# Optimization experiments

Measured on AMD Instinct MI355X. Metric: run time of the kernel, lower is better.

Reference implementation:

```python
import jax, jax.numpy as jnp
import numpy as np

B, H, S, D = 8, 16, 1024, 128

def setup_inputs() -> dict:
    key = jax.random.key(0)
    kq, kk, kv = jax.random.split(key, 3)
    q = jax.random.normal(kq, (B, H, S, D), dtype=jnp.float32)
    k = jax.random.normal(kk, (B, H, S, D), dtype=jnp.float32)
    v = jax.random.normal(kv, (B, H, S, D), dtype=jnp.float32)
    return {"q": q, "k": k, "v": v}

def reference(q, k, v):
    dims = q.shape[-1]
    # scores[..., j, i] = sum_k q[..., j, k] * k_[..., i, k]; note scale is 1/dims (not 1/sqrt(dims))
    scores = jnp.einsum('bhjd,bhid->bhji', q, k) / dims
    probs = jax.nn.softmax(scores, axis=-1)
    out = jnp.einsum('bhji,bhid->bhjd', probs, v)
    return out
```

## Files before the change

### kernel.cpp

```cpp
#include <hip/hip_runtime.h>

#define S_LEN 1024
#define D_DIM 128
#define KVBLK 64
#define QROWS_BLK 128
#define BH_N 128
#define M0_LOG2 2.0f

typedef __attribute__((ext_vector_type(8))) short short8;
typedef __attribute__((ext_vector_type(4))) short short4v;
typedef __attribute__((ext_vector_type(4))) float f32x4;

__device__ __forceinline__ unsigned short f2bf(float f) {
  union { float f; unsigned u; } x; x.f = f;
  unsigned r = x.u + 0x7fffu + ((x.u >> 16) & 1u);
  return (unsigned short)(r >> 16);
}

__device__ __forceinline__ short8 pack8(float4 a, float4 b) {
  short8 f;
  f[0] = (short)f2bf(a.x); f[1] = (short)f2bf(a.y);
  f[2] = (short)f2bf(a.z); f[3] = (short)f2bf(a.w);
  f[4] = (short)f2bf(b.x); f[5] = (short)f2bf(b.y);
  f[6] = (short)f2bf(b.z); f[7] = (short)f2bf(b.w);
  return f;
}

__device__ __forceinline__ void gload_lds16(const void* g, void* l) {
  __builtin_amdgcn_global_load_lds(
      (const __attribute__((address_space(1))) unsigned int*)g,
      (__attribute__((address_space(3))) unsigned int*)l, 16, 0, 0);
}

__global__ __launch_bounds__(256) void conv_k(const float* __restrict__ in,
                                              unsigned short* __restrict__ out,
                                              int n8) {
  int i = blockIdx.x * 256 + threadIdx.x;
  int stride = gridDim.x * 256;
  for (; i < n8; i += stride) {
    float4 a = ((const float4*)in)[i * 2];
    float4 b = ((const float4*)in)[i * 2 + 1];
    ((short8*)out)[i] = pack8(a, b);
  }
}

__global__ __launch_bounds__(256) void conv_vt(const float* __restrict__ v,
                                               unsigned short* __restrict__ vt) {
  __shared__ unsigned short tile[64][72];
  int b = blockIdx.x;
  int d0 = (b & 1) * 64;
  int s0 = ((b >> 1) & 15) * 64;
  int bh = b >> 5;
  int t = threadIdx.x;
  #pragma unroll
  for (int i = 0; i < 4; ++i) {
    int s = (t >> 4) + i * 16;
    int dl = (t & 15) * 4;
    float4 x = *(const float4*)(v + ((size_t)(bh * S_LEN) + s0 + s) * D_DIM + d0 + dl);
    tile[s][dl + 0] = f2bf(x.x); tile[s][dl + 1] = f2bf(x.y);
    tile[s][dl + 2] = f2bf(x.z); tile[s][dl + 3] = f2bf(x.w);
  }
  __syncthreads();
  #pragma unroll
  for (int i = 0; i < 2; ++i) {
    int j = i * 256 + t;
    int dl = j >> 3, sc = j & 7;
    short8 w;
    #pragma unroll
    for (int q = 0; q < 8; ++q) w[q] = (short)tile[sc * 8 + q][dl];
    *(short8*)(vt + ((size_t)(bh * D_DIM) + d0 + dl) * S_LEN + s0 + sc * 8) = w;
  }
}

__global__ __launch_bounds__(512, 4) void attn_main(
    const float* __restrict__ qg, const unsigned short* __restrict__ kbf,
    const unsigned short* __restrict__ vtbf, float* __restrict__ og) {
  __shared__ unsigned short K_lds[2][KVBLK * D_DIM];
  __shared__ unsigned short VT_lds[2][D_DIM * KVBLK];
  __shared__ unsigned short P_lds[8][16 * KVBLK];

  const int tid = threadIdx.x;
  const int lane = tid & 63;
  const int wid = tid >> 6;
  const int l15 = lane & 15;
  const int lg = lane >> 4;

  const int bid = blockIdx.x;
  const int bh = (bid & 7) | ((bid >> 6) << 3);
  const int qt = (bid >> 3) & 7;

  const size_t base = (size_t)bh * (S_LEN * D_DIM);
  const int qw = qt * QROWS_BLK + wid * 16;

  short8 qf[4];
  {
    const float* qp = qg + base + (size_t)(qw + l15) * D_DIM + lg * 8;
    const float s = 0.0078125f * 1.44269504088896f;
    #pragma unroll
    for (int c = 0; c < 4; ++c) {
      float4 a = *(const float4*)(qp + c * 32);
      float4 b = *(const float4*)(qp + c * 32 + 4);
      a.x *= s; a.y *= s; a.z *= s; a.w *= s;
      b.x *= s; b.y *= s; b.z *= s; b.w *= s;
      qf[c] = pack8(a, b);
    }
  }

  float neg_m = -M0_LOG2;
  float l_r = 0.f;
  f32x4 o_acc[8];
  #pragma unroll
  for (int dt = 0; dt < 8; ++dt) o_acc[dt] = (f32x4){0.f, 0.f, 0.f, 0.f};

  const unsigned short* kb = kbf + (size_t)bh * (S_LEN * D_DIM);
  const unsigned short* vtb = vtbf + (size_t)bh * (D_DIM * S_LEN);

  #define STAGE(buf, kv0)                                                      \
    {                                                                          \
      _Pragma("unroll")                                                        \
      for (int i = 0; i < 2; ++i) {                                            \
        int row = wid * 8 + i * 4 + (lane >> 4);                               \
        int c = lane & 15;                                                     \
        const unsigned short* src =                                            \
            kb + (size_t)((kv0) + row) * D_DIM + ((c ^ (row & 7)) * 8);        \
        gload_lds16(src, &K_lds[buf][(wid * 8 + i * 4) * D_DIM]);              \
      }                                                                        \
      _Pragma("unroll")                                                        \
      for (int i = 0; i < 2; ++i) {                                            \
        int drow = wid * 16 + i * 8 + (lane >> 3);                             \
        int c = lane & 7;                                                      \
        const unsigned short* src =                                            \
            vtb + (size_t)drow * S_LEN + (kv0) + ((c ^ (drow & 7)) * 8);       \
        gload_lds16(src, &VT_lds[buf][(wid * 16 + i * 8) * KVBLK]);            \
      }                                                                        \
    }

  STAGE(0, 0);
  __syncthreads();

  char* const pwave = (char*)&P_lds[wid][0];

  #pragma unroll 2
  for (int t = 0; t < S_LEN / KVBLK; ++t) {
    const int cur = t & 1;
    if (t + 1 < S_LEN / KVBLK) STAGE(cur ^ 1, (t + 1) * KVBLK);

    f32x4 sacc[4];
    #pragma unroll
    for (int tc = 0; tc < 4; ++tc) sacc[tc] = (f32x4){neg_m, neg_m, neg_m, neg_m};
    #pragma unroll
    for (int tc = 0; tc < 4; ++tc) {
      int row = tc * 16 + l15;
      #pragma unroll
      for (int ck = 0; ck < 4; ++ck) {
        int sidx = row * 128 + ((ck * 32 + lg * 8) ^ ((row & 7) << 3));
        short8 kf = *(const short8*)&K_lds[cur][sidx];
        sacc[tc] = __builtin_amdgcn_mfma_f32_16x16x32_bf16(kf, qf[ck], sacc[tc], 0, 0, 0);
      }
    }

    float lmax = sacc[0][0];
    #pragma unroll
    for (int tc = 0; tc < 4; ++tc) {
      #pragma unroll
      for (int r = 0; r < 4; ++r) lmax = fmaxf(lmax, sacc[tc][r]);
    }
    if (__any(lmax > 0.f)) {
      float a = lmax;
      a = fmaxf(a, __shfl_xor(a, 16));
      a = fmaxf(a, __shfl_xor(a, 32));
      float delta = fmaxf(a, 0.f);
      neg_m -= delta;
      l_r *= exp2f(-delta);
      float ar[4];
      #pragma unroll
      for (int r = 0; r < 4; ++r)
        ar[r] = exp2f(-__shfl(delta, lg * 4 + r, 16));
      #pragma unroll
      for (int dt = 0; dt < 8; ++dt) {
        #pragma unroll
        for (int r = 0; r < 4; ++r) o_acc[dt][r] *= ar[r];
      }
      #pragma unroll
      for (int tc = 0; tc < 4; ++tc) {
        #pragma unroll
        for (int r = 0; r < 4; ++r) sacc[tc][r] -= delta;
      }
    }

    #pragma unroll
    for (int tc = 0; tc < 4; ++tc) {
      float p0 = exp2f(sacc[tc][0]);
      float p1 = exp2f(sacc[tc][1]);
      float p2 = exp2f(sacc[tc][2]);
      float p3 = exp2f(sacc[tc][3]);
      l_r += (p0 + p1) + (p2 + p3);
      unsigned w0, w1;
      asm("v_cvt_pk_bf16_f32 %0, %1, %2" : "=v"(w0) : "v"(p0), "v"(p1));
      asm("v_cvt_pk_bf16_f32 %0, %1, %2" : "=v"(w1) : "v"(p2), "v"(p3));
      int pb = l15 * 128 + ((tc * 32 + lg * 8) ^ ((l15 & 7) << 4));
      *(uint2*)(pwave + pb) = make_uint2(w0, w1);
    }

    #pragma unroll
    for (int kc = 0; kc < 2; ++kc) {
      int pbr = l15 * 128 + ((kc * 64 + lg * 16) ^ ((l15 & 7) << 4));
      short8 pf = *(const short8*)(pwave + pbr);
      #pragma unroll
      for (int dt = 0; dt < 8; ++dt) {
        int vrow = dt * 16 + l15;
        int vidx = vrow * 64 + ((kc * 32 + lg * 8) ^ ((vrow & 7) << 3));
        short8 vf = *(const short8*)&VT_lds[cur][vidx];
        o_acc[dt] = __builtin_amdgcn_mfma_f32_16x16x32_bf16(pf, vf, o_acc[dt], 0, 0, 0);
      }
    }
    __syncthreads();
  }

  float lsum = l_r;
  lsum += __shfl_xor(lsum, 16);
  lsum += __shfl_xor(lsum, 32);
  float linv = 1.0f / lsum;
  float lr[4];
  #pragma unroll
  for (int r = 0; r < 4; ++r) lr[r] = __shfl(linv, lg * 4 + r, 16);
  #pragma unroll
  for (int r = 0; r < 4; ++r) {
    float* op = og + base + (size_t)(qw + lg * 4 + r) * D_DIM + l15;
    #pragma unroll
    for (int dt = 0; dt < 8; ++dt) op[dt * 16] = o_acc[dt][r] * lr[r];
  }
}

__global__ __launch_bounds__(256) void attn_fused(
    const float* __restrict__ qg, const float* __restrict__ kg,
    const float* __restrict__ vg, float* __restrict__ og) {
  __shared__ unsigned short K_lds[KVBLK * D_DIM];
  __shared__ unsigned short VT_lds[D_DIM * KVBLK];
  __shared__ unsigned short P_lds[4][16 * KVBLK];

  const int tid = threadIdx.x;
  const int lane = tid & 63;
  const int wid = tid >> 6;
  const int l15 = lane & 15;
  const int lg = lane >> 4;

  const int bid = blockIdx.x;
  const int bh = (bid & 7) | ((bid >> 7) << 3);
  const int qt = (bid >> 3) & 15;

  const size_t base = (size_t)bh * (S_LEN * D_DIM);
  const int qw = qt * 64 + wid * 16;

  short8 qf[4];
  {
    const float* qp = qg + base + (size_t)(qw + l15) * D_DIM + lg * 8;
    #pragma unroll
    for (int c = 0; c < 4; ++c) {
      float4 a = *(const float4*)(qp + c * 32);
      float4 b = *(const float4*)(qp + c * 32 + 4);
      const float s = 0.0078125f;
      a.x *= s; a.y *= s; a.z *= s; a.w *= s;
      b.x *= s; b.y *= s; b.z *= s; b.w *= s;
      qf[c] = pack8(a, b);
    }
  }

  float m_r[4], l_r[4];
  f32x4 o_acc[8];
  #pragma unroll
  for (int r = 0; r < 4; ++r) { m_r[r] = -INFINITY; l_r[r] = 0.f; }
  #pragma unroll
  for (int dt = 0; dt < 8; ++dt) o_acc[dt] = (f32x4){0.f, 0.f, 0.f, 0.f};

  for (int kv0 = 0; kv0 < S_LEN; kv0 += KVBLK) {
    {
      const float* kb = kg + base + (size_t)kv0 * D_DIM;
      #pragma unroll
      for (int c = tid; c < KVBLK * D_DIM / 8; c += 256) {
        int row = c >> 4, dc = c & 15;
        const float* p = kb + row * D_DIM + dc * 8;
        float4 a = *(const float4*)p;
        float4 b = *(const float4*)(p + 4);
        int sidx = row * 128 + ((dc * 8) ^ ((row & 7) << 3));
        *(short8*)&K_lds[sidx] = pack8(a, b);
      }
    }
    {
      const float* vb = vg + base + (size_t)kv0 * D_DIM;
      #pragma unroll
      for (int u = tid; u < (KVBLK / 4) * (D_DIM / 4); u += 256) {
        int ib = u & 15;
        int db = u >> 4;
        const float* p = vb + (ib * 4) * D_DIM + db * 4;
        float rr[4][4];
        #pragma unroll
        for (int c = 0; c < 4; ++c) {
          float4 t = *(const float4*)(p + c * D_DIM);
          rr[c][0] = t.x; rr[c][1] = t.y; rr[c][2] = t.z; rr[c][3] = t.w;
        }
        #pragma unroll
        for (int j = 0; j < 4; ++j) {
          short4v w;
          w[0] = (short)f2bf(rr[0][j]); w[1] = (short)f2bf(rr[1][j]);
          w[2] = (short)f2bf(rr[2][j]); w[3] = (short)f2bf(rr[3][j]);
          int row = db * 4 + j;
          int sidx = row * 64 + ((ib * 4) ^ ((row & 7) << 3));
          *(short4v*)&VT_lds[sidx] = w;
        }
      }
    }
    __syncthreads();

    f32x4 sacc[4];
    #pragma unroll
    for (int tc = 0; tc < 4; ++tc) sacc[tc] = (f32x4){0.f, 0.f, 0.f, 0.f};
    #pragma unroll
    for (int tc = 0; tc < 4; ++tc) {
      int row = tc * 16 + l15;
      #pragma unroll
      for (int ck = 0; ck < 4; ++ck) {
        int sidx = row * 128 + ((ck * 32 + lg * 8) ^ ((row & 7) << 3));
        short8 kf = *(const short8*)&K_lds[sidx];
        sacc[tc] = __builtin_amdgcn_mfma_f32_16x16x32_bf16(qf[ck], kf, sacc[tc], 0, 0, 0);
      }
    }

    float alpha[4], ps[4];
    #pragma unroll
    for (int r = 0; r < 4; ++r) {
      float a = fmaxf(fmaxf(sacc[0][r], sacc[1][r]), fmaxf(sacc[2][r], sacc[3][r]));
      a = fmaxf(a, __shfl_xor(a, 1));
      a = fmaxf(a, __shfl_xor(a, 2));
      a = fmaxf(a, __shfl_xor(a, 4));
      a = fmaxf(a, __shfl_xor(a, 8));
      float mn = fmaxf(m_r[r], a);
      alpha[r] = __expf(m_r[r] - mn);
      m_r[r] = mn;
      ps[r] = 0.f;
    }
    #pragma unroll
    for (int tc = 0; tc < 4; ++tc) {
      #pragma unroll
      for (int r = 0; r < 4; ++r) {
        float p = __expf(sacc[tc][r] - m_r[r]);
        ps[r] += p;
        int prow = lg * 4 + r;
        int pcol = tc * 16 + l15;
        P_lds[wid][prow * 64 + (pcol ^ ((prow & 7) << 3))] = f2bf(p);
      }
    }
    #pragma unroll
    for (int r = 0; r < 4; ++r) {
      float s = ps[r];
      s += __shfl_xor(s, 1); s += __shfl_xor(s, 2);
      s += __shfl_xor(s, 4); s += __shfl_xor(s, 8);
      l_r[r] = l_r[r] * alpha[r] + s;
    }
    #pragma unroll
    for (int dt = 0; dt < 8; ++dt) {
      #pragma unroll
      for (int r = 0; r < 4; ++r) o_acc[dt][r] *= alpha[r];
    }

    #pragma unroll
    for (int kc = 0; kc < 2; ++kc) {
      int pidx = l15 * 64 + ((kc * 32 + lg * 8) ^ ((l15 & 7) << 3));
      short8 pf = *(const short8*)&P_lds[wid][pidx];
      #pragma unroll
      for (int dt = 0; dt < 8; ++dt) {
        int vrow = dt * 16 + l15;
        int vidx = vrow * 64 + ((kc * 32 + lg * 8) ^ ((vrow & 7) << 3));
        short8 vf = *(const short8*)&VT_lds[vidx];
        o_acc[dt] = __builtin_amdgcn_mfma_f32_16x16x32_bf16(pf, vf, o_acc[dt], 0, 0, 0);
      }
    }
    __syncthreads();
  }

  #pragma unroll
  for (int r = 0; r < 4; ++r) {
    float inv = 1.0f / l_r[r];
    float* op = og + base + (size_t)(qw + lg * 4 + r) * D_DIM + l15;
    #pragma unroll
    for (int dt = 0; dt < 8; ++dt) op[dt * 16] = o_acc[dt][r] * inv;
  }
}

extern "C" void kernel_launch(void* const* d_in, const int* in_sizes, int n_in,
                              void* d_out, int out_size, void* d_ws, size_t ws_size,
                              hipStream_t stream) {
  const float* q = (const float*)d_in[0];
  const float* k = (const float*)d_in[1];
  const float* v = (const float*)d_in[2];
  float* o = (float*)d_out;

  const size_t n_elem = (size_t)BH_N * S_LEN * D_DIM;
  const size_t need = 2 * n_elem * sizeof(unsigned short);

  if (ws_size >= need) {
    unsigned short* kbf = (unsigned short*)d_ws;
    unsigned short* vtbf = kbf + n_elem;
    conv_k<<<dim3(2048), dim3(256), 0, stream>>>(k, kbf, (int)(n_elem / 8));
    conv_vt<<<dim3(4096), dim3(256), 0, stream>>>(v, vtbf);
    attn_main<<<dim3(1024), dim3(512), 0, stream>>>(q, kbf, vtbf, o);
  } else {
    attn_fused<<<dim3(2048), dim3(256), 0, stream>>>(q, k, v, o);
  }
}
```

Baseline: 136.6 us.

## Switch attention main loop to 32x32x16 MFMA with register-resident P via permlane swap

Rewrites attn_main so each wave handles 32 query rows using 32x32x16 bf16 MFMAs instead of 16 rows with 16x16x32. The probability tile no longer goes through LDS: v_permlane32_swap rearranges the packed bf16 values in registers into the A-operand layout for the PV matmul. Blocks shrink to 256 threads, and s_setprio is raised around MFMA sections. The intent is fewer LDS round-trips and better MFMA efficiency per K/V load, at the cost of higher register pressure per wave and fewer waves per block.

```diff
diff --git a/kernel.cpp b/kernel.cpp
--- a/kernel.cpp
+++ b/kernel.cpp
@@ -3,13 +3,14 @@
 #define S_LEN 1024
 #define D_DIM 128
 #define KVBLK 64
-#define QROWS_BLK 128
 #define BH_N 128
 #define M0_LOG2 2.0f
 
 typedef __attribute__((ext_vector_type(8))) short short8;
 typedef __attribute__((ext_vector_type(4))) short short4v;
 typedef __attribute__((ext_vector_type(4))) float f32x4;
+typedef __attribute__((ext_vector_type(16))) float f32x16;
+typedef __attribute__((ext_vector_type(4))) unsigned int uint4v;
 
 __device__ __forceinline__ unsigned short f2bf(float f) {
   union { float f; unsigned u; } x; x.f = f;
@@ -72,34 +73,33 @@
   }
 }
 
-__global__ __launch_bounds__(512, 4) void attn_main(
+__global__ __launch_bounds__(256, 2) void attn_main(
     const float* __restrict__ qg, const unsigned short* __restrict__ kbf,
     const unsigned short* __restrict__ vtbf, float* __restrict__ og) {
   __shared__ unsigned short K_lds[2][KVBLK * D_DIM];
   __shared__ unsigned short VT_lds[2][D_DIM * KVBLK];
-  __shared__ unsigned short P_lds[8][16 * KVBLK];
 
   const int tid = threadIdx.x;
   const int lane = tid & 63;
   const int wid = tid >> 6;
-  const int l15 = lane & 15;
-  const int lg = lane >> 4;
+  const int l31 = lane & 31;
+  const int hi = lane >> 5;
 
   const int bid = blockIdx.x;
   const int bh = (bid & 7) | ((bid >> 6) << 3);
   const int qt = (bid >> 3) & 7;
 
   const size_t base = (size_t)bh * (S_LEN * D_DIM);
-  const int qw = qt * QROWS_BLK + wid * 16;
-
-  short8 qf[4];
+  const int qw = qt * 128 + wid * 32;
+
+  short8 qf[8];
   {
-    const float* qp = qg + base + (size_t)(qw + l15) * D_DIM + lg * 8;
+    const float* qp = qg + base + (size_t)(qw + l31) * D_DIM + hi * 8;
     const float s = 0.0078125f * 1.44269504088896f;
     #pragma unroll
-    for (int c = 0; c < 4; ++c) {
-      float4 a = *(const float4*)(qp + c * 32);
-      float4 b = *(const float4*)(qp + c * 32 + 4);
+    for (int c = 0; c < 8; ++c) {
+      float4 a = *(const float4*)(qp + c * 16);
+      float4 b = *(const float4*)(qp + c * 16 + 4);
       a.x *= s; a.y *= s; a.z *= s; a.w *= s;
       b.x *= s; b.y *= s; b.z *= s; b.w *= s;
       qf[c] = pack8(a, b);
@@ -108,9 +108,11 @@
 
   float neg_m = -M0_LOG2;
   float l_r = 0.f;
-  f32x4 o_acc[8];
-  #pragma unroll
-  for (int dt = 0; dt < 8; ++dt) o_acc[dt] = (f32x4){0.f, 0.f, 0.f, 0.f};
+  f32x16 o_acc[4];
+  #pragma unroll
+  for (int dt = 0; dt < 4; ++dt)
+    #pragma unroll
+    for (int r = 0; r < 16; ++r) o_acc[dt][r] = 0.f;
 
   const unsigned short* kb = kbf + (size_t)bh * (S_LEN * D_DIM);
   const unsigned short* vtb = vtbf + (size_t)bh * (D_DIM * S_LEN);
@@ -118,117 +120,131 @@
   #define STAGE(buf, kv0)                                                      \
     {                                                                          \
       _Pragma("unroll")                                                        \
-      for (int i = 0; i < 2; ++i) {                                            \
-        int row = wid * 8 + i * 4 + (lane >> 4);                               \
+      for (int i = 0; i < 4; ++i) {                                            \
+        int row = wid * 16 + i * 4 + (lane >> 4);                              \
         int c = lane & 15;                                                     \
         const unsigned short* src =                                            \
             kb + (size_t)((kv0) + row) * D_DIM + ((c ^ (row & 7)) * 8);        \
-        gload_lds16(src, &K_lds[buf][(wid * 8 + i * 4) * D_DIM]);              \
+        gload_lds16(src, &K_lds[buf][(wid * 16 + i * 4) * D_DIM]);             \
       }                                                                        \
       _Pragma("unroll")                                                        \
-      for (int i = 0; i < 2; ++i) {                                            \
-        int drow = wid * 16 + i * 8 + (lane >> 3);                             \
+      for (int i = 0; i < 4; ++i) {                                            \
+        int drow = wid * 32 + i * 8 + (lane >> 3);                             \
         int c = lane & 7;                                                      \
         const unsigned short* src =                                            \
             vtb + (size_t)drow * S_LEN + (kv0) + ((c ^ (drow & 7)) * 8);       \
-        gload_lds16(src, &VT_lds[buf][(wid * 16 + i * 8) * KVBLK]);            \
+        gload_lds16(src, &VT_lds[buf][(wid * 32 + i * 8) * KVBLK]);            \
       }                                                                        \
     }
 
   STAGE(0, 0);
   __syncthreads();
 
-  char* const pwave = (char*)&P_lds[wid][0];
-
-  #pragma unroll 2
   for (int t = 0; t < S_LEN / KVBLK; ++t) {
     const int cur = t & 1;
     if (t + 1 < S_LEN / KVBLK) STAGE(cur ^ 1, (t + 1) * KVBLK);
 
-    f32x4 sacc[4];
-    #pragma unroll
-    for (int tc = 0; tc < 4; ++tc) sacc[tc] = (f32x4){neg_m, neg_m, neg_m, neg_m};
-    #pragma unroll
-    for (int tc = 0; tc < 4; ++tc) {
-      int row = tc * 16 + l15;
-      #pragma unroll
-      for (int ck = 0; ck < 4; ++ck) {
-        int sidx = row * 128 + ((ck * 32 + lg * 8) ^ ((row & 7) << 3));
+    f32x16 sacc[2];
+    #pragma unroll
+    for (int ks = 0; ks < 2; ++ks)
+      #pragma unroll
+      for (int r = 0; r < 16; ++r) sacc[ks][r] = neg_m;
+
+    __builtin_amdgcn_s_setprio(1);
+    #pragma unroll
+    for (int c = 0; c < 8; ++c) {
+      #pragma unroll
+      for (int ks = 0; ks < 2; ++ks) {
+        int row = ks * 32 + l31;
+        int dc = 2 * c + hi;
+        int sidx = row * 128 + ((dc ^ (row & 7)) * 8);
         short8 kf = *(const short8*)&K_lds[cur][sidx];
-        sacc[tc] = __builtin_amdgcn_mfma_f32_16x16x32_bf16(kf, qf[ck], sacc[tc], 0, 0, 0);
-      }
-    }
+        sacc[ks] = __builtin_amdgcn_mfma_f32_32x32x16_bf16(kf, qf[c], sacc[ks], 0, 0, 0);
+      }
+    }
+    __builtin_amdgcn_s_setprio(0);
 
     float lmax = sacc[0][0];
     #pragma unroll
-    for (int tc = 0; tc < 4; ++tc) {
-      #pragma unroll
-      for (int r = 0; r < 4; ++r) lmax = fmaxf(lmax, sacc[tc][r]);
-    }
+    for (int ks = 0; ks < 2; ++ks)
+      #pragma unroll
+      for (int r = 0; r < 16; ++r) lmax = fmaxf(lmax, sacc[ks][r]);
     if (__any(lmax > 0.f)) {
-      float a = lmax;
-      a = fmaxf(a, __shfl_xor(a, 16));
-      a = fmaxf(a, __shfl_xor(a, 32));
+      float a = fmaxf(lmax, __shfl_xor(lmax, 32));
       float delta = fmaxf(a, 0.f);
       neg_m -= delta;
       l_r *= exp2f(-delta);
-      float ar[4];
-      #pragma unroll
-      for (int r = 0; r < 4; ++r)
-        ar[r] = exp2f(-__shfl(delta, lg * 4 + r, 16));
-      #pragma unroll
-      for (int dt = 0; dt < 8; ++dt) {
+      float ar[16];
+      #pragma unroll
+      for (int r = 0; r < 16; ++r)
+        ar[r] = exp2f(-__shfl(delta, (r & 3) + 8 * (r >> 2) + 4 * hi, 64));
+      #pragma unroll
+      for (int dt = 0; dt < 4; ++dt)
         #pragma unroll
-        for (int r = 0; r < 4; ++r) o_acc[dt][r] *= ar[r];
-      }
-      #pragma unroll
-      for (int tc = 0; tc < 4; ++tc) {
+        for (int r = 0; r < 16; ++r) o_acc[dt][r] *= ar[r];
+      #pragma unroll
+      for (int ks = 0; ks < 2; ++ks)
         #pragma unroll
-        for (int r = 0; r < 4; ++r) sacc[tc][r] -= delta;
-      }
-    }
-
-    #pragma unroll
-    for (int tc = 0; tc < 4; ++tc) {
-      float p0 = exp2f(sacc[tc][0]);
-      float p1 = exp2f(sacc[tc][1]);
-      float p2 = exp2f(sacc[tc][2]);
-      float p3 = exp2f(sacc[tc][3]);
-      l_r += (p0 + p1) + (p2 + p3);
-      unsigned w0, w1;
-      asm("v_cvt_pk_bf16_f32 %0, %1, %2" : "=v"(w0) : "v"(p0), "v"(p1));
-      asm("v_cvt_pk_bf16_f32 %0, %1, %2" : "=v"(w1) : "v"(p2), "v"(p3));
-      int pb = l15 * 128 + ((tc * 32 + lg * 8) ^ ((l15 & 7) << 4));
-      *(uint2*)(pwave + pb) = make_uint2(w0, w1);
-    }
-
-    #pragma unroll
-    for (int kc = 0; kc < 2; ++kc) {
-      int pbr = l15 * 128 + ((kc * 64 + lg * 16) ^ ((l15 & 7) << 4));
-      short8 pf = *(const short8*)(pwave + pbr);
-      #pragma unroll
-      for (int dt = 0; dt < 8; ++dt) {
-        int vrow = dt * 16 + l15;
-        int vidx = vrow * 64 + ((kc * 32 + lg * 8) ^ ((vrow & 7) << 3));
-        short8 vf = *(const short8*)&VT_lds[cur][vidx];
-        o_acc[dt] = __builtin_amdgcn_mfma_f32_16x16x32_bf16(pf, vf, o_acc[dt], 0, 0, 0);
+        for (int r = 0; r < 16; ++r) sacc[ks][r] -= delta;
+    }
+
+    #pragma unroll
+    for (int ks = 0; ks < 2; ++ks) {
+      float p[16];
+      #pragma unroll
+      for (int r = 0; r < 16; ++r) p[r] = exp2f(sacc[ks][r]);
+      float s0 = (p[0] + p[1]) + (p[2] + p[3]);
+      float s1 = (p[4] + p[5]) + (p[6] + p[7]);
+      float s2 = (p[8] + p[9]) + (p[10] + p[11]);
+      float s3 = (p[12] + p[13]) + (p[14] + p[15]);
+      l_r += (s0 + s1) + (s2 + s3);
+
+      unsigned w[4][2];
+      #pragma unroll
+      for (int g = 0; g < 4; ++g) {
+        asm("v_cvt_pk_bf16_f32 %0, %1, %2" : "=v"(w[g][0]) : "v"(p[4 * g]), "v"(p[4 * g + 1]));
+        asm("v_cvt_pk_bf16_f32 %0, %1, %2" : "=v"(w[g][1]) : "v"(p[4 * g + 2]), "v"(p[4 * g + 3]));
+      }
+
+      #pragma unroll
+      for (int c = 0; c < 2; ++c) {
+        asm volatile("v_permlane32_swap_b32 %0, %1" : "+v"(w[2 * c][0]), "+v"(w[2 * c + 1][0]));
+        asm volatile("v_permlane32_swap_b32 %0, %1" : "+v"(w[2 * c][1]), "+v"(w[2 * c + 1][1]));
+        uint4v pw;
+        pw[0] = w[2 * c][0];
+        pw[1] = w[2 * c][1];
+        pw[2] = w[2 * c + 1][0];
+        pw[3] = w[2 * c + 1][1];
+        short8 pa = __builtin_bit_cast(short8, pw);
+
+        __builtin_amdgcn_s_setprio(1);
+        #pragma unroll
+        for (int dt = 0; dt < 4; ++dt) {
+          int vrow = dt * 32 + l31;
+          int kc8 = ks * 4 + c * 2 + hi;
+          int vidx = vrow * 64 + ((kc8 ^ (vrow & 7)) * 8);
+          short8 vf = *(const short8*)&VT_lds[cur][vidx];
+          o_acc[dt] = __builtin_amdgcn_mfma_f32_32x32x16_bf16(pa, vf, o_acc[dt], 0, 0, 0);
+        }
+        __builtin_amdgcn_s_setprio(0);
       }
     }
     __syncthreads();
   }
 
-  float lsum = l_r;
-  lsum += __shfl_xor(lsum, 16);
-  lsum += __shfl_xor(lsum, 32);
+  float lsum = l_r + __shfl_xor(l_r, 32);
   float linv = 1.0f / lsum;
-  float lr[4];
-  #pragma unroll
-  for (int r = 0; r < 4; ++r) lr[r] = __shfl(linv, lg * 4 + r, 16);
-  #pragma unroll
-  for (int r = 0; r < 4; ++r) {
-    float* op = og + base + (size_t)(qw + lg * 4 + r) * D_DIM + l15;
-    #pragma unroll
-    for (int dt = 0; dt < 8; ++dt) op[dt * 16] = o_acc[dt][r] * lr[r];
+  float lr16[16];
+  #pragma unroll
+  for (int r = 0; r < 16; ++r)
+    lr16[r] = __shfl(linv, (r & 3) + 8 * (r >> 2) + 4 * hi, 64);
+  #pragma unroll
+  for (int dt = 0; dt < 4; ++dt) {
+    #pragma unroll
+    for (int r = 0; r < 16; ++r) {
+      int qr = (r & 3) + 8 * (r >> 2) + 4 * hi;
+      og[base + (size_t)(qw + qr) * D_DIM + dt * 32 + l31] = o_acc[dt][r] * lr16[r];
+    }
   }
 }
 
@@ -403,7 +419,7 @@
     unsigned short* vtbf = kbf + n_elem;
     conv_k<<<dim3(2048), dim3(256), 0, stream>>>(k, kbf, (int)(n_elem / 8));
     conv_vt<<<dim3(4096), dim3(256), 0, stream>>>(v, vtbf);
-    attn_main<<<dim3(1024), dim3(512), 0, stream>>>(q, kbf, vtbf, o);
+    attn_main<<<dim3(1024), dim3(256), 0, stream>>>(q, kbf, vtbf, o);
   } else {
     attn_fused<<<dim3(2048), dim3(256), 0, stream>>>(q, k, v, o);
   }
```

New measurement: 140.1 us. 2.6% more time.
